# Kernel tuning notes

Hardware: AMD Instinct MI355X
Metric: run time of the kernel (lower is better)

## Reference

```python
import jax, jax.numpy as jnp
import numpy as np

K = 8192        # nodes (radio links)
DEG = 32        # out-degree per node
E = K * DEG
GE = 8          # graph_embedding_size
VAR = np.float32((10.0 ** (-19.9) * 5e6) / 10.0)  # output_noise_power / tx_power


def _init_mlp(key, dims_list):
    # per-node stacked Linear params, torch default init U(-1/sqrt(fan_in), 1/sqrt(fan_in))
    params = []
    for (din, dout) in dims_list:
        key, k1, k2 = jax.random.split(key, 3)
        b = float(1.0 / np.sqrt(din))
        params.append(jax.random.uniform(k1, (K, din, dout), minval=-b, maxval=b, dtype=jnp.float32))
        params.append(jax.random.uniform(k2, (K, dout), minval=-b, maxval=b, dtype=jnp.float32))
    return params


def setup_inputs() -> dict:
    key = jax.random.key(0)
    k = jax.random.split(key, 8)
    # edges sorted by src, exactly DEG distinct non-self out-neighbors per node
    src = jnp.repeat(jnp.arange(K), DEG)
    gaps = jax.random.randint(k[0], (K, DEG), 1, (K - 1) // DEG + 1)
    dst = ((jnp.arange(K)[:, None] + jnp.cumsum(gaps, axis=1)) % K).reshape(-1)
    edge_index = jnp.stack([src, dst])
    x = jax.random.uniform(k[1], (K, 1 + GE), dtype=jnp.float32)
    edge_attr = jax.random.uniform(k[2], (E, 1), dtype=jnp.float32)
    H = jax.random.uniform(k[3], (K, K), dtype=jnp.float32) * 1e-12  # |h_ij|^2 gains
    Wm1, bm1, Wm2, bm2 = _init_mlp(k[4], [(2 + GE, 32), (32, 32)])
    Wu1, bu1, Wu2, bu2 = _init_mlp(k[5], [(33 + GE, 16), (16, GE)])
    Wh1, bh1, Wh2, bh2 = _init_mlp(k[6], [(GE, 16), (16, 1)])
    return dict(x=x, edge_attr=edge_attr, H=H, edge_index=edge_index,
                Wm1=Wm1, bm1=bm1, Wm2=Wm2, bm2=bm2,
                Wu1=Wu1, bu1=bu1, Wu2=Wu2, bu2=bu2,
                Wh1=Wh1, bh1=bh1, Wh2=Wh2, bh2=bh2)


def reference(x, edge_attr, H, edge_index,
              Wm1, bm1, Wm2, bm2, Wu1, bu1, Wu2, bu2, Wh1, bh1, Wh2, bh2):
    src, dst = edge_index[0], edge_index[1]

    def conv(x):
        # message: tmp_e = [x[src_e], edge_attr_e]; node src's private mlp_m.
        # edges are contiguous groups of DEG per src -> grouped GEMM as batched einsum
        tmp = jnp.concatenate([x[src], edge_attr], axis=1).reshape(K, DEG, 2 + GE)
        h = jax.nn.relu(jnp.einsum('ked,kdh->keh', tmp, Wm1) + bm1[:, None])
        msg = jax.nn.relu(jnp.einsum('ked,kdh->keh', h, Wm2) + bm2[:, None])
        aggr = msg.sum(axis=1)                                  # [K,32] sum-aggregate
        t = jnp.concatenate([x, aggr], axis=1)                  # [K,41]
        u = jax.nn.relu(jnp.einsum('kd,kdh->kh', t, Wu1) + bu1)
        comb = jax.nn.relu(jnp.einsum('kd,kdh->kh', u, Wu2) + bu2)  # [K,8]
        return jnp.concatenate([x[:, :1], comb], axis=1)        # keep direct-channel col

    x3 = conv(conv(conv(x)))                                    # 3 rounds of LocalConv
    emb = x3[:, 1:]                                             # [K,8]
    hh = jax.nn.relu(jnp.einsum('kd,kdh->kh', emb, Wh1) + bh1)
    p = jax.nn.sigmoid(jnp.einsum('kd,kdh->kh', hh, Wh2) + bh2)[:, 0]  # power in (0,1)

    # per-node (negative) local rate over 1-hop out-neighborhood
    valid = p * jnp.diagonal(H)                                 # p_i * |h_ii|^2
    interf = jax.ops.segment_sum(p[dst] * H[src, dst], src, num_segments=K) + VAR
    interf = jax.lax.stop_gradient(interf)                      # .detach() in original
    local_rate = -jnp.log2(1.0 + valid / interf)                # [K]
    return local_rate
```

## Files before the change

### kernel.cpp

```cpp
#include <hip/hip_runtime.h>
#include <hip/hip_bf16.h>
#include <math.h>

#define KN 8192
#define DEG 32
#define EE (KN*DEG)

#define VAR_F 6.294627058970831e-15f

typedef __attribute__((ext_vector_type(8)))  short bf16x8;
typedef __attribute__((ext_vector_type(16))) float f32x16;

__device__ __forceinline__ short bf_hi(float f) {
    __hip_bfloat16 h = __float2bfloat16(f);
    return __builtin_bit_cast(short, h);
}
__device__ __forceinline__ float bf_f(short s) {
    __hip_bfloat16 h = __builtin_bit_cast(__hip_bfloat16, s);
    return __bfloat162float(h);
}

__global__ __launch_bounds__(64) void mpnn_fused(
    const float* __restrict__ x,
    const float* __restrict__ edge_attr,
    const float* __restrict__ Wm1, const float* __restrict__ bm1,
    const float* __restrict__ Wm2, const float* __restrict__ bm2,
    const float* __restrict__ Wu1, const float* __restrict__ bu1,
    const float* __restrict__ Wu2, const float* __restrict__ bu2,
    const float* __restrict__ Wh1, const float* __restrict__ bh1,
    const float* __restrict__ Wh2, const float* __restrict__ bh2,
    float* __restrict__ p_out)
{
    __shared__ __align__(16) float c_lds[32];
    __shared__ float xt[44];
    __shared__ float ubuf[16];

    const int lane = threadIdx.x;
    const int col  = lane & 31;
    const int g    = lane >> 5;
    const int k    = blockIdx.x;

    const float a_e = edge_attr[k*32 + col];

    float wm1[9];
    #pragma unroll
    for (int d = 0; d < 9; ++d) wm1[d] = Wm1[k*320 + d*32 + col];
    const float bm1_i = bm1[k*32 + col];
    const float bm2_i = bm2[k*32 + col];

    float w9v[16];
    #pragma unroll
    for (int t = 0; t < 16; ++t) {
        int j = (t >> 3)*16 + g*8 + (t & 7);
        w9v[t] = Wm1[k*320 + 288 + j];
    }

    bf16x8 Bhi[2], Blo[2];
    #pragma unroll
    for (int s = 0; s < 2; ++s) {
        #pragma unroll
        for (int i = 0; i < 8; ++i) {
            int j = s*16 + g*8 + i;
            float wv = Wm2[k*1024 + j*32 + col];
            short h = bf_hi(wv);
            Bhi[s][i] = h;
            Blo[s][i] = bf_hi(wv - bf_f(h));
        }
    }

    const int m  = lane & 15;
    const int dg = lane >> 4;
    float wu1[11];
    #pragma unroll
    for (int t = 0; t < 11; ++t) {
        int d = dg*11 + t;
        wu1[t] = (d < 41) ? Wu1[k*656 + d*16 + m] : 0.f;
    }
    const float bu1_m = bu1[k*16 + m];

    const int o  = lane & 7;
    const int mg = lane >> 3;
    const float wu2a = Wu2[k*128 + (mg*2+0)*8 + o];
    const float wu2b = Wu2[k*128 + (mg*2+1)*8 + o];
    const float bu2_o = bu2[k*8 + o];

    float wh1[8];
    #pragma unroll
    for (int d = 0; d < 8; ++d) wh1[d] = Wh1[k*128 + d*16 + m];
    const float bh1_m = bh1[k*16 + m];
    const float wh2_m = Wh2[k*16 + m];
    const float bh2_k = bh2[k];

    if (lane < 9) xt[lane] = x[k*9 + lane];
    __syncthreads();

    for (int it = 0; it < 3; ++it) {
        float c = bm1_i;
        #pragma unroll
        for (int d = 0; d < 9; ++d) c = fmaf(xt[d], wm1[d], c);
        if (g == 0) c_lds[col] = c;
        __syncthreads();

        const float4* cb = (const float4*)c_lds;
        float4 q0 = cb[g*2 + 0];
        float4 q1 = cb[g*2 + 1];
        float4 q2 = cb[4 + g*2 + 0];
        float4 q3 = cb[4 + g*2 + 1];
        float cv[16] = {q0.x,q0.y,q0.z,q0.w, q1.x,q1.y,q1.z,q1.w,
                        q2.x,q2.y,q2.z,q2.w, q3.x,q3.y,q3.z,q3.w};
        bf16x8 Ahi[2], Alo[2];
        #pragma unroll
        for (int s = 0; s < 2; ++s) {
            #pragma unroll
            for (int i = 0; i < 8; ++i) {
                int t = s*8 + i;
                float hv = fmaxf(fmaf(a_e, w9v[t], cv[t]), 0.f);
                short h = bf_hi(hv);
                Ahi[s][i] = h;
                Alo[s][i] = bf_hi(hv - bf_f(h));
            }
        }

        f32x16 acc;
        #pragma unroll
        for (int r = 0; r < 16; ++r) acc[r] = 0.f;
        #pragma unroll
        for (int s = 0; s < 2; ++s) {
            acc = __builtin_amdgcn_mfma_f32_32x32x16_bf16(Ahi[s], Bhi[s], acc, 0, 0, 0);
            acc = __builtin_amdgcn_mfma_f32_32x32x16_bf16(Ahi[s], Blo[s], acc, 0, 0, 0);
            acc = __builtin_amdgcn_mfma_f32_32x32x16_bf16(Alo[s], Bhi[s], acc, 0, 0, 0);
        }

        float ag = 0.f;
        #pragma unroll
        for (int r = 0; r < 16; ++r) ag += fmaxf(acc[r] + bm2_i, 0.f);
        ag += __shfl_xor(ag, 32);
        __syncthreads();
        if (g == 0) xt[9 + col] = ag;
        __syncthreads();

        float up = 0.f;
        #pragma unroll
        for (int t = 0; t < 11; ++t) {
            int d = dg*11 + t;
            if (d < 41) up = fmaf(xt[d], wu1[t], up);
        }
        up += __shfl_xor(up, 16);
        up += __shfl_xor(up, 32);
        float u = fmaxf(up + bu1_m, 0.f);
        if (lane < 16) ubuf[lane] = u;
        __syncthreads();

        float cp = wu2a * ubuf[mg*2] + wu2b * ubuf[mg*2 + 1];
        cp += __shfl_xor(cp, 8);
        cp += __shfl_xor(cp, 16);
        cp += __shfl_xor(cp, 32);
        float comb = fmaxf(cp + bu2_o, 0.f);
        if (lane < 8) xt[1 + lane] = comb;
        __syncthreads();
    }

    float hp = 0.f;
    #pragma unroll
    for (int d = 0; d < 8; ++d) hp = fmaf(xt[1 + d], wh1[d], hp);
    float hh = fmaxf(hp + bh1_m, 0.f);
    float pp = hh * wh2_m;
    pp += __shfl_xor(pp, 1);
    pp += __shfl_xor(pp, 2);
    pp += __shfl_xor(pp, 4);
    pp += __shfl_xor(pp, 8);
    float z = pp + bh2_k;
    float p = 1.f / (1.f + expf(-z));
    if (lane == 0) p_out[k] = p;
}

__global__ __launch_bounds__(256) void mpnn_interf(
    const float* __restrict__ H,
    const int* __restrict__ edge_index,
    const float* __restrict__ p,
    float* __restrict__ out)
{
    const int t = blockIdx.x * 256 + threadIdx.x;
    const int s = t >> 5;
    const int e = t & 31;
    const int* dst = edge_index + EE;
    const int d = dst[s*DEG + e];
    float part = p[d] * H[(size_t)s*KN + d];
    part += __shfl_xor(part, 1);
    part += __shfl_xor(part, 2);
    part += __shfl_xor(part, 4);
    part += __shfl_xor(part, 8);
    part += __shfl_xor(part, 16);
    if (e == 0) {
        float interf = part + VAR_F;
        float valid  = p[s] * H[(size_t)s*KN + s];
        out[s] = -log1pf(valid / interf) * 1.4426950408889634f;
    }
}

extern "C" void kernel_launch(void* const* d_in, const int* in_sizes, int n_in,
                              void* d_out, int out_size, void* d_ws, size_t ws_size,
                              hipStream_t stream) {
    const float* x         = (const float*)d_in[0];
    const float* edge_attr = (const float*)d_in[1];
    const float* H         = (const float*)d_in[2];
    const int*   edge_idx  = (const int*)  d_in[3];
    const float* Wm1 = (const float*)d_in[4];
    const float* bm1 = (const float*)d_in[5];
    const float* Wm2 = (const float*)d_in[6];
    const float* bm2 = (const float*)d_in[7];
    const float* Wu1 = (const float*)d_in[8];
    const float* bu1 = (const float*)d_in[9];
    const float* Wu2 = (const float*)d_in[10];
    const float* bu2 = (const float*)d_in[11];
    const float* Wh1 = (const float*)d_in[12];
    const float* bh1 = (const float*)d_in[13];
    const float* Wh2 = (const float*)d_in[14];
    const float* bh2 = (const float*)d_in[15];
    float* out = (float*)d_out;
    float* p_ws = (float*)d_ws;

    mpnn_fused<<<KN, 64, 0, stream>>>(x, edge_attr, Wm1, bm1, Wm2, bm2,
                                      Wu1, bu1, Wu2, bu2, Wh1, bh1, Wh2, bh2,
                                      p_ws);
    mpnn_interf<<<(KN*DEG)/256, 256, 0, stream>>>(H, edge_idx, p_ws, out);
}
```

Measured before the change: 31.44 us.

## Pack four nodes per block and stage per-node weights in LDS via float4 loads

```diff
diff --git a/kernel.cpp b/kernel.cpp
--- a/kernel.cpp
+++ b/kernel.cpp
@@ -5,22 +5,23 @@
 #define KN 8192
 #define DEG 32
 #define EE (KN*DEG)
+#define WPB 4
 
 #define VAR_F 6.294627058970831e-15f
 
 typedef __attribute__((ext_vector_type(8)))  short bf16x8;
 typedef __attribute__((ext_vector_type(16))) float f32x16;
 
-__device__ __forceinline__ short bf_hi(float f) {
+static __device__ __forceinline__ short bf_hi(float f) {
     __hip_bfloat16 h = __float2bfloat16(f);
     return __builtin_bit_cast(short, h);
 }
-__device__ __forceinline__ float bf_f(short s) {
+static __device__ __forceinline__ float bf_f(short s) {
     __hip_bfloat16 h = __builtin_bit_cast(__hip_bfloat16, s);
     return __bfloat162float(h);
 }
 
-__global__ __launch_bounds__(64) void mpnn_fused(
+__global__ __launch_bounds__(256, 4) void mpnn_fused(
     const float* __restrict__ x,
     const float* __restrict__ edge_attr,
     const float* __restrict__ Wm1, const float* __restrict__ bm1,
@@ -31,29 +32,51 @@
     const float* __restrict__ Wh2, const float* __restrict__ bh2,
     float* __restrict__ p_out)
 {
-    __shared__ __align__(16) float c_lds[32];
-    __shared__ float xt[44];
-    __shared__ float ubuf[16];
-
-    const int lane = threadIdx.x;
+    __shared__ __align__(16) float wlds[WPB][1360];
+    __shared__ __align__(16) float c_lds[WPB][32];
+    __shared__ float xt[WPB][44];
+    __shared__ float ubuf[WPB][16];
+
+    const int w    = threadIdx.x >> 6;
+    const int lane = threadIdx.x & 63;
     const int col  = lane & 31;
     const int g    = lane >> 5;
-    const int k    = blockIdx.x;
+    const int k    = blockIdx.x * WPB + w;
+    float* WL = wlds[w];
+
+    enum { O_WM1 = 0,    O_WU1 = 320,  O_WH1 = 976,  O_WU2 = 1104,
+           O_BM1 = 1232, O_BM2 = 1264, O_BU1 = 1296, O_BU2 = 1312,
+           O_BH1 = 1320, O_WH2 = 1336, O_BH2 = 1352 };
+
+    {
+        const float4* s4 = (const float4*)(Wm1 + (size_t)k*320);
+        float4* d4 = (float4*)(WL + O_WM1);
+        d4[lane] = s4[lane];
+        if (lane < 16) d4[64+lane] = s4[64+lane];
+
+        s4 = (const float4*)(Wu1 + (size_t)k*656);
+        d4 = (float4*)(WL + O_WU1);
+        d4[lane]    = s4[lane];
+        d4[64+lane] = s4[64+lane];
+        if (lane < 36) d4[128+lane] = s4[128+lane];
+
+        if (lane < 32)
+            ((float4*)(WL + O_WH1))[lane]    = ((const float4*)(Wh1 + (size_t)k*128))[lane];
+        else
+            ((float4*)(WL + O_WU2))[lane-32] = ((const float4*)(Wu2 + (size_t)k*128))[lane-32];
+
+        if      (lane <  8) ((float4*)(WL + O_BM1))[lane]    = ((const float4*)(bm1 + (size_t)k*32))[lane];
+        else if (lane < 16) ((float4*)(WL + O_BM2))[lane- 8] = ((const float4*)(bm2 + (size_t)k*32))[lane-8];
+        else if (lane < 20) ((float4*)(WL + O_BU1))[lane-16] = ((const float4*)(bu1 + (size_t)k*16))[lane-16];
+        else if (lane < 22) ((float4*)(WL + O_BU2))[lane-20] = ((const float4*)(bu2 + (size_t)k*8 ))[lane-20];
+        else if (lane < 26) ((float4*)(WL + O_BH1))[lane-22] = ((const float4*)(bh1 + (size_t)k*16))[lane-22];
+        else if (lane < 30) ((float4*)(WL + O_WH2))[lane-26] = ((const float4*)(Wh2 + (size_t)k*16))[lane-26];
+        else if (lane == 30) WL[O_BH2] = bh2[k];
+
+        if (lane >= 40 && lane < 49) xt[w][lane-40] = x[(size_t)k*9 + lane - 40];
+    }
 
     const float a_e = edge_attr[k*32 + col];
-
-    float wm1[9];
-    #pragma unroll
-    for (int d = 0; d < 9; ++d) wm1[d] = Wm1[k*320 + d*32 + col];
-    const float bm1_i = bm1[k*32 + col];
-    const float bm2_i = bm2[k*32 + col];
-
-    float w9v[16];
-    #pragma unroll
-    for (int t = 0; t < 16; ++t) {
-        int j = (t >> 3)*16 + g*8 + (t & 7);
-        w9v[t] = Wm1[k*320 + 288 + j];
-    }
 
     bf16x8 Bhi[2], Blo[2];
     #pragma unroll
@@ -61,47 +84,30 @@
         #pragma unroll
         for (int i = 0; i < 8; ++i) {
             int j = s*16 + g*8 + i;
-            float wv = Wm2[k*1024 + j*32 + col];
+            float wv = Wm2[(size_t)k*1024 + j*32 + col];
             short h = bf_hi(wv);
             Bhi[s][i] = h;
             Blo[s][i] = bf_hi(wv - bf_f(h));
         }
     }
 
+    __syncthreads();
+
+    const float bm1_i = WL[O_BM1 + col];
+    const float bm2_i = WL[O_BM2 + col];
     const int m  = lane & 15;
     const int dg = lane >> 4;
-    float wu1[11];
-    #pragma unroll
-    for (int t = 0; t < 11; ++t) {
-        int d = dg*11 + t;
-        wu1[t] = (d < 41) ? Wu1[k*656 + d*16 + m] : 0.f;
-    }
-    const float bu1_m = bu1[k*16 + m];
-
     const int o  = lane & 7;
     const int mg = lane >> 3;
-    const float wu2a = Wu2[k*128 + (mg*2+0)*8 + o];
-    const float wu2b = Wu2[k*128 + (mg*2+1)*8 + o];
-    const float bu2_o = bu2[k*8 + o];
-
-    float wh1[8];
-    #pragma unroll
-    for (int d = 0; d < 8; ++d) wh1[d] = Wh1[k*128 + d*16 + m];
-    const float bh1_m = bh1[k*16 + m];
-    const float wh2_m = Wh2[k*16 + m];
-    const float bh2_k = bh2[k];
-
-    if (lane < 9) xt[lane] = x[k*9 + lane];
-    __syncthreads();
 
     for (int it = 0; it < 3; ++it) {
         float c = bm1_i;
         #pragma unroll
-        for (int d = 0; d < 9; ++d) c = fmaf(xt[d], wm1[d], c);
-        if (g == 0) c_lds[col] = c;
-        __syncthreads();
-
-        const float4* cb = (const float4*)c_lds;
+        for (int d = 0; d < 9; ++d) c = fmaf(xt[w][d], WL[O_WM1 + d*32 + col], c);
+        if (g == 0) c_lds[w][col] = c;
+        __syncthreads();
+
+        const float4* cb = (const float4*)c_lds[w];
         float4 q0 = cb[g*2 + 0];
         float4 q1 = cb[g*2 + 1];
         float4 q2 = cb[4 + g*2 + 0];
@@ -114,7 +120,8 @@
             #pragma unroll
             for (int i = 0; i < 8; ++i) {
                 int t = s*8 + i;
-                float hv = fmaxf(fmaf(a_e, w9v[t], cv[t]), 0.f);
+                float w9 = WL[O_WM1 + 288 + (s*16 + g*8 + i)];
+                float hv = fmaxf(fmaf(a_e, w9, cv[t]), 0.f);
                 short h = bf_hi(hv);
                 Ahi[s][i] = h;
                 Alo[s][i] = bf_hi(hv - bf_f(h));
@@ -135,41 +142,41 @@
         #pragma unroll
         for (int r = 0; r < 16; ++r) ag += fmaxf(acc[r] + bm2_i, 0.f);
         ag += __shfl_xor(ag, 32);
-        __syncthreads();
-        if (g == 0) xt[9 + col] = ag;
+        if (g == 0) xt[w][9 + col] = ag;
         __syncthreads();
 
         float up = 0.f;
         #pragma unroll
         for (int t = 0; t < 11; ++t) {
             int d = dg*11 + t;
-            if (d < 41) up = fmaf(xt[d], wu1[t], up);
+            if (d < 41) up = fmaf(xt[w][d], WL[O_WU1 + d*16 + m], up);
         }
         up += __shfl_xor(up, 16);
         up += __shfl_xor(up, 32);
-        float u = fmaxf(up + bu1_m, 0.f);
-        if (lane < 16) ubuf[lane] = u;
-        __syncthreads();
-
-        float cp = wu2a * ubuf[mg*2] + wu2b * ubuf[mg*2 + 1];
+        float u = fmaxf(up + WL[O_BU1 + m], 0.f);
+        if (lane < 16) ubuf[w][lane] = u;
+        __syncthreads();
+
+        float cp = WL[O_WU2 + (mg*2+0)*8 + o] * ubuf[w][mg*2]
+                 + WL[O_WU2 + (mg*2+1)*8 + o] * ubuf[w][mg*2+1];
         cp += __shfl_xor(cp, 8);
         cp += __shfl_xor(cp, 16);
         cp += __shfl_xor(cp, 32);
-        float comb = fmaxf(cp + bu2_o, 0.f);
-        if (lane < 8) xt[1 + lane] = comb;
+        float comb = fmaxf(cp + WL[O_BU2 + o], 0.f);
+        if (lane < 8) xt[w][1 + lane] = comb;
         __syncthreads();
     }
 
     float hp = 0.f;
     #pragma unroll
-    for (int d = 0; d < 8; ++d) hp = fmaf(xt[1 + d], wh1[d], hp);
-    float hh = fmaxf(hp + bh1_m, 0.f);
-    float pp = hh * wh2_m;
+    for (int d = 0; d < 8; ++d) hp = fmaf(xt[w][1 + d], WL[O_WH1 + d*16 + m], hp);
+    float hh = fmaxf(hp + WL[O_BH1 + m], 0.f);
+    float pp = hh * WL[O_WH2 + m];
     pp += __shfl_xor(pp, 1);
     pp += __shfl_xor(pp, 2);
     pp += __shfl_xor(pp, 4);
     pp += __shfl_xor(pp, 8);
-    float z = pp + bh2_k;
+    float z = pp + WL[O_BH2];
     float p = 1.f / (1.f + expf(-z));
     if (lane == 0) p_out[k] = p;
 }
@@ -220,8 +227,8 @@
     float* out = (float*)d_out;
     float* p_ws = (float*)d_ws;
 
-    mpnn_fused<<<KN, 64, 0, stream>>>(x, edge_attr, Wm1, bm1, Wm2, bm2,
-                                      Wu1, bu1, Wu2, bu2, Wh1, bh1, Wh2, bh2,
-                                      p_ws);
+    mpnn_fused<<<KN/WPB, 256, 0, stream>>>(x, edge_attr, Wm1, bm1, Wm2, bm2,
+                                           Wu1, bu1, Wu2, bu2, Wh1, bh1, Wh2, bh2,
+                                           p_ws);
     mpnn_interf<<<(KN*DEG)/256, 256, 0, stream>>>(H, edge_idx, p_ws, out);
 }
```

After: 37.79 us. 20.2% more time.
